# Optimization experiments

Hardware: AMD Instinct MI355X
Metric: run time of the kernel (lower is better)

The kernel has to match this reference:

```python
import jax, jax.numpy as jnp
from jax import lax
import numpy as np

DIM, K, OUT_DIM = 128, 64, 256
SAMPLE_STEP = 30  # eval mode
WIN = 200


def _l2n(v, axis):
    return v / jnp.maximum(jnp.linalg.norm(v, axis=axis, keepdims=True), 1e-12)


def _conv(x, w, b, pad):
    y = lax.conv_general_dilated(x, w, (1, 1), [(pad, pad), (pad, pad)],
                                 dimension_numbers=('NCHW', 'OIHW', 'NCHW'))
    return y + b[None, :, None, None]


def _maxpool(x, kh, kw, sh, sw, ph, pw):
    return lax.reduce_window(x, -jnp.inf, lax.max, (1, 1, kh, kw), (1, 1, sh, sw),
                             [(0, 0), (0, 0), (ph, ph), (pw, pw)])


def setup_inputs() -> dict:
    key = jax.random.key(0)
    ks = jax.random.split(key, 12)
    s = 1.0 / np.sqrt(DIM)
    return {
        'x': jax.random.normal(ks[0], (4, DIM, 48, 900), jnp.float32),
        'cluster_centers': jax.random.uniform(ks[1], (K, DIM), jnp.float32) * s,
        'conv_w': jax.random.normal(ks[2], (K, DIM), jnp.float32) * s * 0.1,
        'conv_b': jax.random.normal(ks[3], (K,), jnp.float32) * s * 0.1,
        'w1': jax.random.normal(ks[4], (2 * DIM, DIM, 5, 5), jnp.float32) * 0.02,
        'b1': jnp.zeros((2 * DIM,), jnp.float32),
        'w2': jax.random.normal(ks[5], (4 * DIM, 2 * DIM, 5, 5), jnp.float32) * 0.01,
        'b2': jnp.zeros((4 * DIM,), jnp.float32),
        'w3': jax.random.normal(ks[6], (8 * DIM, 4 * DIM, 5, 5), jnp.float32) * 0.01,
        'b3': jnp.zeros((8 * DIM,), jnp.float32),
        'mlp_w': jax.random.normal(ks[7], (OUT_DIM, DIM * (K + 8)), jnp.float32) * s * 0.01,
        'mlp_b': jax.random.normal(ks[8], (OUT_DIM,), jnp.float32) * s * 0.01,
    }


def reference(x, cluster_centers, conv_w, conv_b, w1, b1, w2, b2, w3, b3, mlp_w, mlp_b):
    N, C, H, W = x.shape  # (4, 128, 48, 900)
    # ---- soft assignment (1x1 conv), softmax over clusters ----
    logits = jnp.einsum('nchw,kc->nkhw', x, conv_w) + conv_b[None, :, None, None]
    a = jax.nn.softmax(logits, axis=1)  # softmax over K (per spatial pos)
    # ---- residual-weighted sum over H, fused (avoids (N,K,C,HW) tensor) ----
    # sum_h a[n,k,h,w] * (x[n,c,h,w] - centers[k,c])
    xa = jnp.einsum('nkhw,nchw->nkcw', a, x)
    a_sum = a.sum(axis=2)  # (N,K,W)
    res = xa - cluster_centers[None, :, :, None] * a_sum[:, :, None, :]  # (N,K,C,W)
    # ---- x_conv feature branch on circularly padded input ----
    xp = jnp.concatenate([x[..., 800:], x, x[..., :100]], axis=-1)  # (N,C,H,1100)
    h = jax.nn.leaky_relu(_conv(xp, w1, b1, 2), 0.2)
    h = _maxpool(h, 3, 3, 3, 1, 0, 1)          # (N,256,16,1100)
    h = jax.nn.leaky_relu(_conv(h, w2, b2, 2), 0.2)
    h = _maxpool(h, 4, 5, 4, 1, 0, 2)          # (N,512,4,1100)
    h = _conv(h, w3, b3, 2)
    h = _maxpool(h, 4, WIN, 4, 1, 0, 0)        # (N,1024,1,901)
    xf = h[:, :, 0, ::SAMPLE_STEP][..., :-1]   # (N,1024,30)
    xf = _l2n(jnp.transpose(xf, (0, 2, 1)), axis=2)  # (N,30,1024)
    n_win = xf.shape[1]
    # ---- windowed VLAD pooling via cumsum (equiv to unfold(200, step).sum) ----
    resp = jnp.concatenate([res[..., 800:], res, res[..., :100]], axis=-1)  # (N,K,C,1100)
    cs = jnp.concatenate([jnp.zeros_like(resp[..., :1]), jnp.cumsum(resp, axis=-1)], axis=-1)
    starts = jnp.arange(n_win) * SAMPLE_STEP  # last window dropped, matching [:-1]
    vlad = cs[..., starts + WIN] - cs[..., starts]  # (N,K,C,30)
    vlad = jnp.transpose(vlad, (0, 3, 1, 2))        # (N,30,K,C)
    vlad = _l2n(vlad, axis=3)                        # intra-norm per cluster
    vlad = _l2n(vlad.reshape(N * n_win, K * C), axis=1)
    feat = jnp.concatenate([vlad, xf.reshape(N * n_win, -1)], axis=1)  # (N*30, 9216)
    out = _l2n(feat @ mlp_w.T + mlp_b, axis=1)
    return out.reshape(N, n_win, -1)
```

## Files before the change

### kernel.cpp

```cpp
#include <hip/hip_runtime.h>
#include <hip/hip_bf16.h>

#define NB   4
#define DIM  128
#define KC   64
#define HH   48
#define WW   900
#define WPAD 1100
#define WST  1160
#define NT   30
#define OC1  256
#define OC2  512
#define OC3  1024

typedef __attribute__((ext_vector_type(8))) short bf16x8;
typedef __attribute__((ext_vector_type(4))) float f32x4;
typedef unsigned short u16;
typedef unsigned int u32;

__device__ __forceinline__ u16 f2bf(float f){
  __hip_bfloat16 h = __float2bfloat16(f);
  u16 u; __builtin_memcpy(&u, &h, 2); return u;
}
__device__ __forceinline__ float bf2f(u16 u){
  __hip_bfloat16 h; __builtin_memcpy(&h, &u, 2); return __bfloat162float(h);
}

typedef __attribute__((address_space(1))) const u32 g_u32;
typedef __attribute__((address_space(3))) u32 l_u32;
__device__ __forceinline__ void gll16(const void* g, void* l){
  __builtin_amdgcn_global_load_lds((g_u32*)g, (l_u32*)l, 16, 0, 0);
}


__global__ __launch_bounds__(256) void transpose_xt(const float* __restrict__ x, float* __restrict__ xt){
  __shared__ float tile[32][33];
  int n = blockIdx.z;
  int r0 = blockIdx.y*32, w0 = blockIdx.x*32;
  int t = threadIdx.x;
  int tr = t >> 5, tc = t & 31;
  #pragma unroll
  for (int i = 0; i < 4; ++i){
    int r = r0 + tr + i*8, w = w0 + tc;
    tile[tr + i*8][tc] = (w < WW) ? x[((size_t)n*(DIM*HH) + r)*WW + w] : 0.f;
  }
  __syncthreads();
  #pragma unroll
  for (int i = 0; i < 4; ++i){
    int w = w0 + tr + i*8, r = r0 + tc;
    if (w < WW) xt[((size_t)n*WW + w)*(DIM*HH) + r] = tile[tc][tr + i*8];
  }
}

__global__ __launch_bounds__(256) void vlad_softmax(const float* __restrict__ x,
    const float* __restrict__ conv_w, const float* __restrict__ conv_b, float* __restrict__ a){
  __shared__ float cwT[DIM*KC];
  __shared__ float cbs[KC];
  int t = threadIdx.x;
  for (int i = t; i < DIM*KC; i += 256){ int c = i >> 6, k = i & 63; cwT[i] = conv_w[k*DIM + c]; }
  if (t < KC) cbs[t] = conv_b[t];
  __syncthreads();
  int w = blockIdx.x*256 + t, h = blockIdx.y, n = blockIdx.z;
  bool ok = (w < WW);
  float lg[KC];
  #pragma unroll
  for (int k = 0; k < KC; ++k) lg[k] = cbs[k];
  const float* xp = x + (size_t)n*DIM*HH*WW + (size_t)h*WW + (ok ? w : 0);
  for (int c = 0; c < DIM; ++c){
    float xv = ok ? xp[(size_t)c*HH*WW] : 0.f;
    const float* cw = &cwT[c*KC];
    #pragma unroll
    for (int k = 0; k < KC; ++k) lg[k] += xv * cw[k];
  }
  float m = lg[0];
  #pragma unroll
  for (int k = 1; k < KC; ++k) m = fmaxf(m, lg[k]);
  float s = 0.f;
  #pragma unroll
  for (int k = 0; k < KC; ++k){ lg[k] = __expf(lg[k]-m); s += lg[k]; }
  float inv = 1.f/s;
  if (ok){
    float* dst = a + (((size_t)(n*HH + h))*WW + w)*KC;
    #pragma unroll
    for (int k = 0; k < KC; k += 4){
      float4 v = make_float4(lg[k]*inv, lg[k+1]*inv, lg[k+2]*inv, lg[k+3]*inv);
      *(float4*)&dst[k] = v;
    }
  }
}

__global__ __launch_bounds__(256) void vlad_xa2(const float* __restrict__ xt, const float* __restrict__ a,
    const float* __restrict__ centers, float* __restrict__ ps){
  __shared__ float aT[HH][KC];
  __shared__ float xT[DIM*HH];
  int t = threadIdx.x, s = blockIdx.x, n = blockIdx.y;
  int k = t >> 2, cb4 = t & 3;
  float acc[32];
  #pragma unroll
  for (int j = 0; j < 32; ++j) acc[j] = 0.f;
  float Sacc = 0.f;
  for (int i = 0; i < 10; ++i){
    int p = s*10 + i;
    int w = (p < 100) ? p + 800 : ((p < 1000) ? p - 100 : p - 1000);
    for (int e = t; e < HH*KC; e += 256){
      int h = e >> 6, kk = e & 63;
      aT[h][kk] = a[(((size_t)(n*HH + h))*WW + w)*KC + kk];
    }
    {
      const float4* src = (const float4*)(xt + ((size_t)n*WW + w)*(DIM*HH));
      float4* dst4 = (float4*)xT;
      for (int e = t; e < (DIM*HH)/4; e += 256) dst4[e] = src[e];
    }
    __syncthreads();
    float areg[HH];
    #pragma unroll
    for (int h = 0; h < HH; ++h) areg[h] = aT[h][k];
    float Sw = 0.f;
    #pragma unroll
    for (int h = 0; h < HH; ++h) Sw += areg[h];
    Sacc += Sw;
    #pragma unroll 2
    for (int j = 0; j < 32; ++j){
      const float4* xr = (const float4*)&xT[(cb4 + 4*j)*HH];
      float sum = 0.f;
      #pragma unroll
      for (int h4 = 0; h4 < HH/4; ++h4){
        float4 xv = xr[h4];
        sum += areg[h4*4+0]*xv.x + areg[h4*4+1]*xv.y + areg[h4*4+2]*xv.z + areg[h4*4+3]*xv.w;
      }
      acc[j] += sum;
    }
    __syncthreads();
  }
  const float* ck = centers + (size_t)k*DIM;
  float* dst = ps + (((size_t)(n*KC + k))*110 + s)*DIM;
  #pragma unroll
  for (int j = 0; j < 32; ++j){
    int c = cb4 + 4*j;
    dst[c] = acc[j] - ck[c]*Sacc;
  }
}

__global__ __launch_bounds__(128) void vlad_win2(const float* __restrict__ ps, float* __restrict__ vlad){
  int c = threadIdx.x, k = blockIdx.x, tt = blockIdx.y, n = blockIdx.z;
  const float* base = ps + ((size_t)(n*KC + k))*110*DIM + c;
  float v = 0.f;
  #pragma unroll
  for (int u = 0; u < 20; ++u) v += base[(3*tt + u)*DIM];
  float ss = v*v;
  #pragma unroll
  for (int m = 1; m < 64; m <<= 1) ss += __shfl_xor(ss, m);
  __shared__ float red[2];
  if ((c & 63) == 0) red[c >> 6] = ss;
  __syncthreads();
  float tot = red[0] + red[1];
  float inv = 1.f / fmaxf(sqrtf(tot), 1e-12f);
  vlad[(((size_t)(n*NT + tt))*KC + k)*DIM + c] = v*inv;
}

__global__ __launch_bounds__(256) void vlad_gnorm(float* __restrict__ vlad){
  int row = blockIdx.x, t = threadIdx.x;
  float4* v = (float4*)(vlad + (size_t)row*(KC*DIM));
  float4 r[8]; float ss = 0.f;
  #pragma unroll
  for (int i = 0; i < 8; ++i){
    r[i] = v[t + i*256];
    ss += r[i].x*r[i].x + r[i].y*r[i].y + r[i].z*r[i].z + r[i].w*r[i].w;
  }
  #pragma unroll
  for (int m = 1; m < 64; m <<= 1) ss += __shfl_xor(ss, m);
  __shared__ float red[4];
  if ((t & 63) == 0) red[t >> 6] = ss;
  __syncthreads();
  float tot = red[0]+red[1]+red[2]+red[3];
  float inv = 1.f / fmaxf(sqrtf(tot), 1e-12f);
  #pragma unroll
  for (int i = 0; i < 8; ++i){
    float4 o = r[i]; o.x*=inv; o.y*=inv; o.z*=inv; o.w*=inv;
    v[t + i*256] = o;
  }
}


__global__ __launch_bounds__(256) void build_xpb(const float* __restrict__ x, u16* __restrict__ xpb){
  __shared__ u16 tile[DIM][33];
  int t = threadIdx.x, h = blockIdx.y, n = blockIdx.z;
  int b0 = blockIdx.x*32;
  #pragma unroll
  for (int i = 0; i < 16; ++i){
    int e = t + i*256;
    int c = e >> 5, bl = e & 31;
    int b = b0 + bl, w = b - 2;
    float v = 0.f;
    if (w >= 0 && w < WPAD){
      int wsrc = (w + 800) % 900;
      v = x[((size_t)(n*DIM + c)*HH + h)*WW + wsrc];
    }
    tile[c][bl] = f2bf(v);
  }
  __syncthreads();
  #pragma unroll
  for (int i = 0; i < 16; ++i){
    int e = t + i*256;
    int bl = e >> 7, c = e & 127;
    int b = b0 + bl;
    if (b < WST) xpb[((size_t)(n*HH + h)*WST + b)*DIM + c] = tile[c][bl];
  }
}

__global__ __launch_bounds__(256) void pack_w(const float* __restrict__ w, u16* __restrict__ wp, int OC, int IC){
  int idx = blockIdx.x*256 + threadIdx.x;
  int total = OC*IC*25;
  if (idx >= total) return;
  int ic = idx % IC; int r = idx / IC; int oc = r % OC; int tap = r / OC;
  wp[idx] = f2bf(w[((size_t)oc*IC + ic)*25 + tap]);
}

template<int IC, int OC, int H>
__global__ __launch_bounds__(256,2) void conv5x5(const u16* __restrict__ in, const u16* __restrict__ wp,
    const float* __restrict__ bias, u16* __restrict__ out){
  constexpr int NICB = IC/128;
  __shared__ u16 sIn[132*128];
  __shared__ u16 sW[128*128];
  int t = threadIdx.x;
  int wave = t >> 6, lane = t & 63, lr = lane & 15, lgp = lane >> 4;
  int w0  = blockIdx.x * 128;
  int ocb = blockIdx.y * 128;
  int nh = blockIdx.z; int n = nh / H, h = nh % H;
  int wo_oc = (wave & 1)*64, wo_w = (wave >> 1)*64;
  f32x4 acc[4][4] = {};
  const u16* inN = in + (size_t)n*H*WST*IC;
  for (int dh = 0; dh < 5; ++dh){
    int hin = h + dh - 2;
    if (hin < 0 || hin >= H) continue;
    const u16* rowbase = inN + (size_t)hin*WST*IC;
    for (int icb = 0; icb < NICB; ++icb){
      __syncthreads();
      for (int i = wave; i < 33; i += 4){
        int qq = i*64 + lane;
        int r = qq >> 4, cp = qq & 15;
        int c = cp ^ (r & 7);
        gll16(rowbase + (size_t)(w0 + r)*IC + icb*128 + c*8, &sIn[i*512]);
      }
      for (int dw = 0; dw < 5; ++dw){
        if (dw) __syncthreads();
        {
          int tap = dh*5 + dw;
          const u16* wsrc = wp + ((size_t)tap*OC + ocb)*IC + (size_t)icb*128;
          for (int i = wave; i < 32; i += 4){
            int qq = i*64 + lane;
            int r = qq >> 4, cp = qq & 15;
            int c = cp ^ (r & 7);
            gll16(wsrc + (size_t)r*IC + c*8, &sW[i*512]);
          }
        }
        __syncthreads();
        __builtin_amdgcn_s_setprio(1);
        #pragma unroll
        for (int k0i = 0; k0i < 4; ++k0i){
          bf16x8 A[4], B[4];
          #pragma unroll
          for (int j = 0; j < 4; ++j){
            int ar = wo_oc + j*16 + lr;
            A[j] = *(const bf16x8*)&sW[ar*128 + (((k0i*4 + lgp) ^ (lr & 7)) << 3)];
            int br = wo_w + j*16 + lr + dw;
            B[j] = *(const bf16x8*)&sIn[br*128 + (((k0i*4 + lgp) ^ (br & 7)) << 3)];
          }
          #pragma unroll
          for (int ja = 0; ja < 4; ++ja)
            #pragma unroll
            for (int jb = 0; jb < 4; ++jb)
              acc[ja][jb] = __builtin_amdgcn_mfma_f32_16x16x32_bf16(A[ja], B[jb], acc[ja][jb], 0, 0, 0);
        }
        __builtin_amdgcn_s_setprio(0);
      }
    }
  }
  u16* outP = out + ((size_t)(n*H + h)*WST + 2)*OC;
  #pragma unroll
  for (int ja = 0; ja < 4; ++ja){
    int oc = ocb + wo_oc + ja*16 + lgp*4;
    float4 bv = *(const float4*)&bias[oc];
    #pragma unroll
    for (int jb = 0; jb < 4; ++jb){
      int wg = w0 + wo_w + jb*16 + lr;
      if (wg < WPAD){
        f32x4 av = acc[ja][jb];
        ushort4 o;
        o.x = f2bf(av[0] + bv.x);
        o.y = f2bf(av[1] + bv.y);
        o.z = f2bf(av[2] + bv.z);
        o.w = f2bf(av[3] + bv.w);
        *(ushort4*)(outP + (size_t)wg*OC + oc) = o;
      }
    }
  }
}

__global__ __launch_bounds__(256) void pool1k(const u16* __restrict__ in, u16* __restrict__ out){
  int t = threadIdx.x;
  int wb = blockIdx.x*4 + (t >> 6);
  int oc = (t & 63)*4;
  int ho = blockIdx.y, n = blockIdx.z;
  int wo = wb - 2;
  float m0=0.f,m1=0.f,m2=0.f,m3=0.f;
  if (wo >= 0 && wo < WPAD){
    m0=m1=m2=m3=-1e30f;
    #pragma unroll
    for (int kh = 0; kh < 3; ++kh){
      const u16* row = in + ((size_t)(n*HH + ho*3 + kh)*WST + 2)*OC1 + oc;
      #pragma unroll
      for (int kw = 0; kw < 3; ++kw){
        int wi = wo - 1 + kw;
        if (wi >= 0 && wi < WPAD){
          ushort4 v = *(const ushort4*)(row + (size_t)wi*OC1);
          m0 = fmaxf(m0, bf2f(v.x)); m1 = fmaxf(m1, bf2f(v.y));
          m2 = fmaxf(m2, bf2f(v.z)); m3 = fmaxf(m3, bf2f(v.w));
        }
      }
    }
    m0 = (m0>0.f)?m0:0.2f*m0; m1 = (m1>0.f)?m1:0.2f*m1;
    m2 = (m2>0.f)?m2:0.2f*m2; m3 = (m3>0.f)?m3:0.2f*m3;
  }
  ushort4 o; o.x=f2bf(m0); o.y=f2bf(m1); o.z=f2bf(m2); o.w=f2bf(m3);
  *(ushort4*)(out + ((size_t)(n*16 + ho)*WST + wb)*OC1 + oc) = o;
}

__global__ __launch_bounds__(256) void pool2k(const u16* __restrict__ in, u16* __restrict__ out){
  int t = threadIdx.x;
  int wb = blockIdx.x*2 + (t >> 7);
  int oc = (t & 127)*4;
  int ho = blockIdx.y, n = blockIdx.z;
  int wo = wb - 2;
  float m0=0.f,m1=0.f,m2=0.f,m3=0.f;
  if (wo >= 0 && wo < WPAD){
    m0=m1=m2=m3=-1e30f;
    #pragma unroll
    for (int kh = 0; kh < 4; ++kh){
      const u16* row = in + ((size_t)(n*16 + ho*4 + kh)*WST + 2)*OC2 + oc;
      #pragma unroll
      for (int kw = 0; kw < 5; ++kw){
        int wi = wo - 2 + kw;
        if (wi >= 0 && wi < WPAD){
          ushort4 v = *(const ushort4*)(row + (size_t)wi*OC2);
          m0 = fmaxf(m0, bf2f(v.x)); m1 = fmaxf(m1, bf2f(v.y));
          m2 = fmaxf(m2, bf2f(v.z)); m3 = fmaxf(m3, bf2f(v.w));
        }
      }
    }
    m0 = (m0>0.f)?m0:0.2f*m0; m1 = (m1>0.f)?m1:0.2f*m1;
    m2 = (m2>0.f)?m2:0.2f*m2; m3 = (m3>0.f)?m3:0.2f*m3;
  }
  ushort4 o; o.x=f2bf(m0); o.y=f2bf(m1); o.z=f2bf(m2); o.w=f2bf(m3);
  *(ushort4*)(out + ((size_t)(n*4 + ho)*WST + wb)*OC2 + oc) = o;
}

__global__ __launch_bounds__(256) void pool3k(const u16* __restrict__ in, float* __restrict__ xfraw){
  int tt = blockIdx.x, hh = blockIdx.y, n = blockIdx.z;
  int oc = threadIdx.x*4;
  float m0=-1e30f,m1=-1e30f,m2=-1e30f,m3=-1e30f;
  const u16* row = in + ((size_t)(n*4 + hh)*WST + 2 + 30*tt)*OC3 + oc;
  for (int p = 0; p < 200; ++p){
    ushort4 v = *(const ushort4*)(row + (size_t)p*OC3);
    m0 = fmaxf(m0, bf2f(v.x)); m1 = fmaxf(m1, bf2f(v.y));
    m2 = fmaxf(m2, bf2f(v.z)); m3 = fmaxf(m3, bf2f(v.w));
  }
  float* dst = xfraw + (((size_t)(n*NT + tt))*4 + hh)*OC3 + oc;
  dst[0]=m0; dst[1]=m1; dst[2]=m2; dst[3]=m3;
}

__global__ __launch_bounds__(256) void xf_norm(const float* __restrict__ xfraw, float* __restrict__ xf){
  int row = blockIdx.x, t = threadIdx.x;
  const float* src = xfraw + (size_t)row*4096;
  float v[4]; float ss = 0.f;
  #pragma unroll
  for (int j = 0; j < 4; ++j){
    float m = src[t + j*256];
    #pragma unroll
    for (int hh = 1; hh < 4; ++hh) m = fmaxf(m, src[hh*1024 + t + j*256]);
    v[j] = m; ss += m*m;
  }
  #pragma unroll
  for (int m = 1; m < 64; m <<= 1) ss += __shfl_xor(ss, m);
  __shared__ float red[4];
  if ((t & 63) == 0) red[t >> 6] = ss;
  __syncthreads();
  float tot = red[0]+red[1]+red[2]+red[3];
  float inv = 1.f/fmaxf(sqrtf(tot), 1e-12f);
  float* dst = xf + (size_t)row*OC3;
  #pragma unroll
  for (int j = 0; j < 4; ++j) dst[t + j*256] = v[j]*inv;
}

__global__ __launch_bounds__(256) void mlp_part(const float* __restrict__ vlad, const float* __restrict__ xf,
    const float* __restrict__ W, float* __restrict__ part){
  __shared__ float feat[4][256];
  int kc = blockIdx.x, rb = blockIdx.y, t = threadIdx.x;
  int i0 = kc*256;
  #pragma unroll
  for (int r = 0; r < 4; ++r){
    int row = rb*4 + r;
    int i = i0 + t;
    feat[r][t] = (i < 8192) ? vlad[(size_t)row*8192 + i] : xf[(size_t)row*1024 + (i - 8192)];
  }
  __syncthreads();
  const float* wr = W + (size_t)t*9216 + i0;
  float a0=0.f, a1=0.f, a2=0.f, a3=0.f;
  for (int i = 0; i < 256; i += 4){
    float4 wv = *(const float4*)&wr[i];
    a0 += feat[0][i]*wv.x + feat[0][i+1]*wv.y + feat[0][i+2]*wv.z + feat[0][i+3]*wv.w;
    a1 += feat[1][i]*wv.x + feat[1][i+1]*wv.y + feat[1][i+2]*wv.z + feat[1][i+3]*wv.w;
    a2 += feat[2][i]*wv.x + feat[2][i+1]*wv.y + feat[2][i+2]*wv.z + feat[2][i+3]*wv.w;
    a3 += feat[3][i]*wv.x + feat[3][i+1]*wv.y + feat[3][i+2]*wv.z + feat[3][i+3]*wv.w;
  }
  float* p0 = part + (((size_t)(rb*4 + 0)*36 + kc))*256 + t;
  p0[0]          = a0;
  p0[36*256]     = a1;
  p0[2*36*256]   = a2;
  p0[3*36*256]   = a3;
}

__global__ __launch_bounds__(256) void mlp_reduce(const float* __restrict__ part, const float* __restrict__ b,
    float* __restrict__ out){
  int row = blockIdx.x, t = threadIdx.x;
  const float* pr = part + (size_t)row*36*256 + t;
  float acc = b[t];
  #pragma unroll
  for (int kc = 0; kc < 36; ++kc) acc += pr[kc*256];
  float ss = acc*acc;
  #pragma unroll
  for (int m = 1; m < 64; m <<= 1) ss += __shfl_xor(ss, m);
  __shared__ float red[4];
  if ((t & 63) == 0) red[t >> 6] = ss;
  __syncthreads();
  float tot = red[0]+red[1]+red[2]+red[3];
  float inv = 1.f/fmaxf(sqrtf(tot), 1e-12f);
  out[(size_t)row*256 + t] = acc*inv;
}

extern "C" void kernel_launch(void* const* d_in, const int* in_sizes, int n_in,
                              void* d_out, int out_size, void* d_ws, size_t ws_size,
                              hipStream_t stream){
  const float* x       = (const float*)d_in[0];
  const float* centers = (const float*)d_in[1];
  const float* conv_w  = (const float*)d_in[2];
  const float* conv_b  = (const float*)d_in[3];
  const float* w1      = (const float*)d_in[4];
  const float* b1      = (const float*)d_in[5];
  const float* w2      = (const float*)d_in[6];
  const float* b2      = (const float*)d_in[7];
  const float* w3      = (const float*)d_in[8];
  const float* b3      = (const float*)d_in[9];
  const float* mlp_w   = (const float*)d_in[10];
  const float* mlp_b   = (const float*)d_in[11];
  float* out = (float*)d_out;
  char* ws = (char*)d_ws;
  const size_t MB = 1ull << 20;
  if (ws_size < 248*MB) return;

  float* vlad  = (float*)(ws + 0);
  float* xf    = (float*)(ws + 4*MB);
  float* xfraw = (float*)(ws + 5*MB);
  char*  AR    = ws + 7*MB;
  float* xt = (float*)(AR + 0);
  float* a  = (float*)(AR + 85*MB);
  float* ps = (float*)(AR + 128*MB);
  u16* xpb = (u16*)(AR + 0);
  u16* wp1 = (u16*)(AR + 55*MB);
  u16* wp2 = (u16*)(AR + 57*MB);
  u16* wp3 = (u16*)(AR + 64*MB);
  u16* h1  = (u16*)(AR + 89*MB);
  u16* p1  = (u16*)(AR + 0);
  u16* h2  = (u16*)(AR + 89*MB);
  u16* p2  = (u16*)(AR + 163*MB);
  u16* h3  = (u16*)(AR + 0);
  float* part = (float*)(AR + 200*MB);

  transpose_xt<<<dim3(29,192,NB), 256, 0, stream>>>(x, xt);
  vlad_softmax<<<dim3(4,HH,NB), 256, 0, stream>>>(x, conv_w, conv_b, a);
  vlad_xa2<<<dim3(110,NB), 256, 0, stream>>>(xt, a, centers, ps);
  vlad_win2<<<dim3(KC,NT,NB), 128, 0, stream>>>(ps, vlad);
  vlad_gnorm<<<dim3(NB*NT), 256, 0, stream>>>(vlad);

  pack_w<<<dim3(3200),  256, 0, stream>>>(w1, wp1, OC1, DIM);
  pack_w<<<dim3(12800), 256, 0, stream>>>(w2, wp2, OC2, OC1);
  pack_w<<<dim3(51200), 256, 0, stream>>>(w3, wp3, OC3, OC2);
  build_xpb<<<dim3(37,HH,NB), 256, 0, stream>>>(x, xpb);
  conv5x5<128,256,48><<<dim3(9, OC1/128, NB*HH), 256, 0, stream>>>(xpb, wp1, b1, h1);
  pool1k<<<dim3(WST/4,16,NB), 256, 0, stream>>>(h1, p1);
  conv5x5<256,512,16><<<dim3(9, OC2/128, NB*16), 256, 0, stream>>>(p1, wp2, b2, h2);
  pool2k<<<dim3(WST/2,4,NB), 256, 0, stream>>>(h2, p2);
  conv5x5<512,1024,4><<<dim3(9, OC3/128, NB*4), 256, 0, stream>>>(p2, wp3, b3, h3);
  pool3k<<<dim3(NT,4,NB), 256, 0, stream>>>(h3, xfraw);
  xf_norm<<<dim3(NB*NT), 256, 0, stream>>>(xfraw, xf);

  mlp_part<<<dim3(36,30), 256, 0, stream>>>(vlad, xf, mlp_w, part);
  mlp_reduce<<<dim3(NB*NT), 256, 0, stream>>>(part, mlp_b, out);
}
```

Measured before the change: 1.848 ms.

## Load conv weights directly from global in MFMA-fragment layout, widen OC tile

Weights are now packed into a layout that matches the MFMA A-fragment order, so each wave reads its A operands straight from global memory (L2/L1) instead of staging them through shared memory. This drops the per-tap weight LDS load and its five barriers per input block. Each block now covers 256 output channels with each wave owning 64 OCs across all 128 widths, which doubles the accumulator registers to 128 floats per thread. The costs are higher register pressure, which may hurt occupancy, half as many blocks, and global-memory latency on the weight loads inside the MFMA loop.

```diff
diff --git a/kernel.cpp b/kernel.cpp
--- a/kernel.cpp
+++ b/kernel.cpp
@@ -208,11 +208,18 @@
   }
 }
 
-__global__ __launch_bounds__(256) void pack_w(const float* __restrict__ w, u16* __restrict__ wp, int OC, int IC){
+__global__ __launch_bounds__(256) void pack_w2(const float* __restrict__ w, u16* __restrict__ wp,
+    int OC, int IC, int NICB){
   int idx = blockIdx.x*256 + threadIdx.x;
   int total = OC*IC*25;
   if (idx >= total) return;
-  int ic = idx % IC; int r = idx / IC; int oc = r % OC; int tap = r / OC;
+  int e = idx & 7;
+  int q = idx >> 3;
+  int oc = q % OC;  int q2 = q / OC;
+  int lgp = q2 & 3; int k0i = (q2 >> 2) & 3;
+  int q3 = q2 >> 4;
+  int icb = q3 % NICB; int tap = q3 / NICB;
+  int ic = icb*128 + k0i*32 + lgp*8 + e;
   wp[idx] = f2bf(w[((size_t)oc*IC + ic)*25 + tap]);
 }
 
@@ -221,14 +228,13 @@
     const float* __restrict__ bias, u16* __restrict__ out){
   constexpr int NICB = IC/128;
   __shared__ u16 sIn[132*128];
-  __shared__ u16 sW[128*128];
   int t = threadIdx.x;
   int wave = t >> 6, lane = t & 63, lr = lane & 15, lgp = lane >> 4;
   int w0  = blockIdx.x * 128;
-  int ocb = blockIdx.y * 128;
+  int ocb = blockIdx.y * 256;
   int nh = blockIdx.z; int n = nh / H, h = nh % H;
-  int wo_oc = (wave & 1)*64, wo_w = (wave >> 1)*64;
-  f32x4 acc[4][4] = {};
+  int wo_oc = wave*64;
+  f32x4 acc[4][8] = {};
   const u16* inN = in + (size_t)n*H*WST*IC;
   for (int dh = 0; dh < 5; ++dh){
     int hin = h + dh - 2;
@@ -242,34 +248,27 @@
         int c = cp ^ (r & 7);
         gll16(rowbase + (size_t)(w0 + r)*IC + icb*128 + c*8, &sIn[i*512]);
       }
+      __syncthreads();
+      #pragma unroll
       for (int dw = 0; dw < 5; ++dw){
-        if (dw) __syncthreads();
-        {
-          int tap = dh*5 + dw;
-          const u16* wsrc = wp + ((size_t)tap*OC + ocb)*IC + (size_t)icb*128;
-          for (int i = wave; i < 32; i += 4){
-            int qq = i*64 + lane;
-            int r = qq >> 4, cp = qq & 15;
-            int c = cp ^ (r & 7);
-            gll16(wsrc + (size_t)r*IC + c*8, &sW[i*512]);
-          }
-        }
-        __syncthreads();
+        int tap = dh*5 + dw;
+        const u16* wtap = wp + (size_t)(tap*NICB + icb)*16*OC*8;
         __builtin_amdgcn_s_setprio(1);
         #pragma unroll
         for (int k0i = 0; k0i < 4; ++k0i){
-          bf16x8 A[4], B[4];
+          const u16* apan = wtap + (size_t)(k0i*4 + lgp)*OC*8 + (size_t)(ocb + wo_oc + lr)*8;
+          bf16x8 A[4], B[8];
           #pragma unroll
-          for (int j = 0; j < 4; ++j){
-            int ar = wo_oc + j*16 + lr;
-            A[j] = *(const bf16x8*)&sW[ar*128 + (((k0i*4 + lgp) ^ (lr & 7)) << 3)];
-            int br = wo_w + j*16 + lr + dw;
-            B[j] = *(const bf16x8*)&sIn[br*128 + (((k0i*4 + lgp) ^ (br & 7)) << 3)];
+          for (int ja = 0; ja < 4; ++ja) A[ja] = *(const bf16x8*)(apan + ja*16*8);
+          #pragma unroll
+          for (int jb = 0; jb < 8; ++jb){
+            int br = jb*16 + lr + dw;
+            B[jb] = *(const bf16x8*)&sIn[br*128 + (((k0i*4 + lgp) ^ (br & 7)) << 3)];
           }
           #pragma unroll
           for (int ja = 0; ja < 4; ++ja)
             #pragma unroll
-            for (int jb = 0; jb < 4; ++jb)
+            for (int jb = 0; jb < 8; ++jb)
               acc[ja][jb] = __builtin_amdgcn_mfma_f32_16x16x32_bf16(A[ja], B[jb], acc[ja][jb], 0, 0, 0);
         }
         __builtin_amdgcn_s_setprio(0);
@@ -282,8 +281,8 @@
     int oc = ocb + wo_oc + ja*16 + lgp*4;
     float4 bv = *(const float4*)&bias[oc];
     #pragma unroll
-    for (int jb = 0; jb < 4; ++jb){
-      int wg = w0 + wo_w + jb*16 + lr;
+    for (int jb = 0; jb < 8; ++jb){
+      int wg = w0 + jb*16 + lr;
       if (wg < WPAD){
         f32x4 av = acc[ja][jb];
         ushort4 o;
@@ -482,15 +481,15 @@
   vlad_win2<<<dim3(KC,NT,NB), 128, 0, stream>>>(ps, vlad);
   vlad_gnorm<<<dim3(NB*NT), 256, 0, stream>>>(vlad);
 
-  pack_w<<<dim3(3200),  256, 0, stream>>>(w1, wp1, OC1, DIM);
-  pack_w<<<dim3(12800), 256, 0, stream>>>(w2, wp2, OC2, OC1);
-  pack_w<<<dim3(51200), 256, 0, stream>>>(w3, wp3, OC3, OC2);
+  pack_w2<<<dim3(3200),  256, 0, stream>>>(w1, wp1, OC1, DIM, 1);
+  pack_w2<<<dim3(12800), 256, 0, stream>>>(w2, wp2, OC2, OC1, 2);
+  pack_w2<<<dim3(51200), 256, 0, stream>>>(w3, wp3, OC3, OC2, 4);
   build_xpb<<<dim3(37,HH,NB), 256, 0, stream>>>(x, xpb);
-  conv5x5<128,256,48><<<dim3(9, OC1/128, NB*HH), 256, 0, stream>>>(xpb, wp1, b1, h1);
+  conv5x5<128,256,48><<<dim3(9, OC1/256, NB*HH), 256, 0, stream>>>(xpb, wp1, b1, h1);
   pool1k<<<dim3(WST/4,16,NB), 256, 0, stream>>>(h1, p1);
-  conv5x5<256,512,16><<<dim3(9, OC2/128, NB*16), 256, 0, stream>>>(p1, wp2, b2, h2);
+  conv5x5<256,512,16><<<dim3(9, OC2/256, NB*16), 256, 0, stream>>>(p1, wp2, b2, h2);
   pool2k<<<dim3(WST/2,4,NB), 256, 0, stream>>>(h2, p2);
-  conv5x5<512,1024,4><<<dim3(9, OC3/128, NB*4), 256, 0, stream>>>(p2, wp3, b3, h3);
+  conv5x5<512,1024,4><<<dim3(9, OC3/256, NB*4), 256, 0, stream>>>(p2, wp3, b3, h3);
   pool3k<<<dim3(NT,4,NB), 256, 0, stream>>>(h3, xfraw);
   xf_norm<<<dim3(NB*NT), 256, 0, stream>>>(xfraw, xf);
 
```

Measured after the change: 1.891 ms. 1.02x slower.
